# Performance work log

Measured on AMD Instinct MI355X. Metric: run time of the kernel, lower is better.

The kernel has to match this reference:

```python
import jax, jax.numpy as jnp
import numpy as np

N_NODES = 100000
N_EDGES = 1600000
IN_DIM, HID_DIM, OUT_DIM = 128, 128, 40
EPS = 1e-12


def setup_inputs() -> dict:
    key = jax.random.key(0)
    ks = jax.random.split(key, 7)
    x = jax.random.normal(ks[0], (N_NODES, IN_DIM), dtype=jnp.float32)
    edge_index = jax.random.randint(ks[1], (2, N_EDGES), 0, N_NODES, dtype=jnp.int64)
    s1 = 1.0 / np.sqrt(IN_DIM)
    s2 = 1.0 / np.sqrt(HID_DIM)
    return {
        "x": x,
        "edge_index": edge_index,
        "W1_l": jax.random.normal(ks[2], (HID_DIM, IN_DIM), dtype=jnp.float32) * s1,
        "b1": jnp.zeros((HID_DIM,), dtype=jnp.float32),
        "W1_r": jax.random.normal(ks[3], (HID_DIM, IN_DIM), dtype=jnp.float32) * s1,
        "W2_l": jax.random.normal(ks[4], (OUT_DIM, HID_DIM), dtype=jnp.float32) * s2,
        "b2": jnp.zeros((OUT_DIM,), dtype=jnp.float32),
        "W2_r": jax.random.normal(ks[5], (OUT_DIM, HID_DIM), dtype=jnp.float32) * s2,
    }


def _mean_aggregate(x, src, dst, deg_inv):
    # gather source features, scatter-sum into destination nodes, divide by degree
    summed = jax.ops.segment_sum(x[src], dst, num_segments=N_NODES)  # [N, d]
    return summed * deg_inv[:, None]


def _sage_conv(x, src, dst, deg_inv, W_l, b_l, W_r):
    # PyG SAGEConv(mean, normalize=True): lin_l(mean(x_j)) + lin_r(x_i), then L2-normalize
    agg = _mean_aggregate(x, src, dst, deg_inv)
    out = agg @ W_l.T + b_l + x @ W_r.T
    norm = jnp.sqrt(jnp.sum(out * out, axis=-1, keepdims=True))
    return out / jnp.maximum(norm, EPS)


def reference(x, edge_index, W1_l, b1, W1_r, W2_l, b2, W2_r):
    src, dst = edge_index[0], edge_index[1]
    deg = jax.ops.segment_sum(jnp.ones((src.shape[0],), dtype=x.dtype), dst,
                              num_segments=N_NODES)
    deg_inv = 1.0 / jnp.maximum(deg, 1.0)

    h = _sage_conv(x, src, dst, deg_inv, W1_l, b1, W1_r)
    h = jax.nn.relu(h)  # dropout = identity (deterministic reference)
    h = _sage_conv(h, src, dst, deg_inv, W2_l, b2, W2_r)
    h = jax.nn.relu(h)
    return jax.nn.log_softmax(h, axis=-1)
```

## Files before the change

### kernel.cpp

```cpp
#include <hip/hip_runtime.h>
#include <hip/hip_bf16.h>

#define N_NODES 100000
#define N_EDGES 1600000
#define IN_DIM 128
#define HID_DIM 128
#define OUT_DIM 40

#define BSHIFT 9
#define NBUCK 196
#define CHUNK 4096
#define NCHUNK ((N_EDGES + CHUNK - 1) / CHUNK)

typedef __attribute__((ext_vector_type(8))) short short8;
typedef __attribute__((ext_vector_type(4))) float float4v;
typedef __attribute__((ext_vector_type(2))) float f32x2;
typedef __attribute__((ext_vector_type(2))) unsigned int u32x2;
typedef __attribute__((ext_vector_type(4))) unsigned int u32x4;

typedef unsigned char u8;
typedef unsigned short u16;
typedef unsigned int u32;
typedef unsigned long long u64;

__device__ __forceinline__ float bflo(u32 v) { union { u32 u; float f; } c; c.u = v << 16; return c.f; }
__device__ __forceinline__ float bfhi(u32 v) { union { u32 u; float f; } c; c.u = v & 0xffff0000u; return c.f; }
__device__ __forceinline__ u16 f2bf(float f) {
    union { float f; u32 u; } c; c.f = f;
    u32 r = c.u + 0x7fffu + ((c.u >> 16) & 1u);
    return (u16)(r >> 16);
}
__device__ __forceinline__ u32 pk(float lo, float hi) {
    return ((u32)f2bf(hi) << 16) | (u32)f2bf(lo);
}

__device__ __forceinline__ u32 f2fp8(float f) {
    union { float f; u32 u; } c; c.f = f;
    u32 s = (c.u >> 24) & 0x80u;
    u32 a = c.u & 0x7fffffffu;
    u32 code;
    if (a >= 0x3C800000u) {
        if (a > 0x43E00000u) a = 0x43E00000u;
        u32 r = a + 0x0007FFFFu + ((a >> 20) & 1u);
        code = (((r >> 23) - 120u) << 3) | ((r >> 20) & 7u);
        if (code > 0x7Eu) code = 0x7Eu;
    } else {
        union { u32 u; float f; } d; d.u = a;
        code = (u32)(int)rintf(d.f * 512.0f);
    }
    return s | code;
}


#define XBLKS ((N_NODES * IN_DIM / 4 + 255) / 256)
#define WTRIP1 2048
#define WTRIP2 768
#define WBLKS 22

__global__ __launch_bounds__(256) void k_cvtall(
    const float* __restrict__ x, u16* __restrict__ xb, u32* __restrict__ xb8,
    const float* __restrict__ w1l, const float* __restrict__ w1r,
    const float* __restrict__ w2l, const float* __restrict__ w2r,
    u16* __restrict__ w1lf, u16* __restrict__ w1rf,
    u16* __restrict__ w2lf, u16* __restrict__ w2rf,
    const int* __restrict__ idx, int* __restrict__ bucket_size) {
    __shared__ int cnt[NBUCK];
    int b = blockIdx.x;
    if (b < XBLKS) {
        int i = b * 256 + threadIdx.x;
        if (i < N_NODES * IN_DIM / 4) {
            float4v v = reinterpret_cast<const float4v*>(x)[i];
            u32x2 o;
            o.x = pk(v.x, v.y);
            o.y = pk(v.z, v.w);
            reinterpret_cast<u32x2*>(xb)[i] = o;
            xb8[i] = f2fp8(v.x) | (f2fp8(v.y) << 8) | (f2fp8(v.z) << 16) | (f2fp8(v.w) << 24);
        }
        return;
    }
    if (b < XBLKS + WBLKS) {
        int i = (b - XBLKS) * 256 + threadIdx.x;
        const float* s; u16* d; int t; int rows;
        if (i < WTRIP1)            { s = w1l; d = w1lf; t = i;                 rows = HID_DIM; }
        else if (i < 2*WTRIP1)     { s = w1r; d = w1rf; t = i - WTRIP1;        rows = HID_DIM; }
        else if (i < 2*WTRIP1+WTRIP2)   { s = w2l; d = w2lf; t = i - 2*WTRIP1; rows = OUT_DIM; }
        else if (i < 2*WTRIP1+2*WTRIP2) { s = w2r; d = w2rf; t = i - 2*WTRIP1-WTRIP2; rows = OUT_DIM; }
        else return;
        int lane = t & 63;
        int ks = (t >> 6) & 3;
        int ct = t >> 8;
        int row = ct * 16 + (lane & 15);
        int col = ks * 32 + (lane >> 4) * 8;
        u32x4 o;
        if (row < rows) {
            const float* sp = s + row * 128 + col;
            float4v v0 = *reinterpret_cast<const float4v*>(sp);
            float4v v1 = *reinterpret_cast<const float4v*>(sp + 4);
            o.x = pk(v0.x, v0.y); o.y = pk(v0.z, v0.w);
            o.z = pk(v1.x, v1.y); o.w = pk(v1.z, v1.w);
        } else { o.x = 0; o.y = 0; o.z = 0; o.w = 0; }
        reinterpret_cast<u32x4*>(d)[t] = o;
        return;
    }
    int t = threadIdx.x;
    for (int i = t; i < NBUCK; i += 256) cnt[i] = 0;
    __syncthreads();
    int base = (b - XBLKS - WBLKS) * CHUNK;
    int n = min(CHUNK, N_EDGES - base);
    for (int i = t; i < n; i += 256)
        atomicAdd(&cnt[idx[N_EDGES + base + i] >> BSHIFT], 1);
    __syncthreads();
    for (int i = t; i < NBUCK; i += 256)
        if (cnt[i]) atomicAdd(&bucket_size[i], cnt[i]);
}


__global__ __launch_bounds__(1024) void k_bscatter(const int* __restrict__ idx,
                                                   const int* __restrict__ bucket_size,
                                                   int* __restrict__ bucket_cur,
                                                   u64* __restrict__ rec) {
    __shared__ int cnt[NBUCK], gbase[NBUCK];
    __shared__ int sa[256], sb[256];
    int t = threadIdx.x;
    const int nt = 1024;
    for (int i = t; i < NBUCK; i += nt) cnt[i] = 0;
    __syncthreads();
    int base = blockIdx.x * CHUNK;
    int n = min(CHUNK, N_EDGES - base);
    int eb[4], eq[4];
    u64 er[4];
    #pragma unroll
    for (int k = 0; k < 4; ++k) {
        int i = t + k * nt;
        if (i < n) {
            int srcv = idx[base + i];
            int dstv = idx[N_EDGES + base + i];
            int b = dstv >> BSHIFT;
            eb[k] = b;
            eq[k] = atomicAdd(&cnt[b], 1);
            er[k] = ((u64)(u32)dstv << 32) | (u32)srcv;
        }
    }
    int myv = 0;
    if (t < 256) {
        myv = (t < NBUCK) ? bucket_size[t] : 0;
        sa[t] = myv;
    }
    __syncthreads();
    int *s = sa, *d = sb;
    for (int dd = 1; dd < 256; dd <<= 1) {
        if (t < 256) d[t] = s[t] + ((t >= dd) ? s[t - dd] : 0);
        __syncthreads();
        int* tm = s; s = d; d = tm;
    }
    if (t < NBUCK) {
        int v = cnt[t];
        gbase[t] = v ? (s[t] - myv) + atomicAdd(&bucket_cur[t], v) : 0;
    }
    __syncthreads();
    #pragma unroll
    for (int k = 0; k < 4; ++k) {
        int i = t + k * nt;
        if (i < n) rec[gbase[eb[k]] + eq[k]] = er[k];
    }
}

__global__ __launch_bounds__(1024) void k_bfill(const u64* __restrict__ rec,
                                                const int* __restrict__ bucket_size,
                                                int* __restrict__ row_start,
                                                int* __restrict__ csr) {
    __shared__ int deg[512], cur[512];
    __shared__ int sa[512], sb[512];
    int t = threadIdx.x;
    int nt = blockDim.x;
    int b = blockIdx.x;
    int node0 = b << BSHIFT;
    int nn = min(512, N_NODES - node0);
    int esz = bucket_size[b];
    if (t < 256) sa[t] = (t < NBUCK) ? bucket_size[t] : 0;
    __syncthreads();
    {
        int *s = sa, *d = sb;
        for (int dd = 1; dd < 256; dd <<= 1) {
            if (t < 256) d[t] = s[t] + ((t >= dd) ? s[t - dd] : 0);
            __syncthreads();
            int* tm = s; s = d; d = tm;
        }
        if (t == 0) cur[0] = s[b] - esz;
    }
    __syncthreads();
    int ebase = cur[0];
    __syncthreads();
    for (int i = t; i < 512; i += nt) deg[i] = 0;
    __syncthreads();
    for (int i = t; i < esz; i += nt)
        atomicAdd(&deg[((int)(rec[ebase + i] >> 32)) & 511], 1);
    __syncthreads();
    for (int i = t; i < 512; i += nt) sa[i] = deg[i];
    __syncthreads();
    int *s = sa, *d = sb;
    for (int dd = 1; dd < 512; dd <<= 1) {
        for (int i = t; i < 512; i += nt) d[i] = s[i] + ((i >= dd) ? s[i - dd] : 0);
        __syncthreads();
        int* tm = s; s = d; d = tm;
    }
    for (int i = t; i < 512; i += nt) {
        int excl = s[i] - deg[i];
        cur[i] = excl;
        if (i < nn) row_start[node0 + i] = ebase + excl;
    }
    if (b == NBUCK - 1 && t == 0) row_start[N_NODES] = N_EDGES;
    __syncthreads();
    for (int i = t; i < esz; i += nt) {
        u64 r = rec[ebase + i];
        int dl = ((int)(r >> 32)) & 511;
        int p = atomicAdd(&cur[dl], 1);
        csr[ebase + p] = (int)(r & 0xffffffffu);
    }
}


__global__ void k_agg(const u32x2* __restrict__ fp,
                      const int* __restrict__ csr,
                      const int* __restrict__ row_start,
                      u16* __restrict__ agg) {
    int lane = threadIdx.x & 63;
    int wave = threadIdx.x >> 6;
    int sub = lane >> 4;
    int li = lane & 15;
    int n = blockIdx.x * 16 + wave * 4 + sub;
    int s = row_start[n];
    int e = row_start[n + 1];
    f32x2 ac0 = {0.f, 0.f}, ac1 = {0.f, 0.f}, ac2 = {0.f, 0.f}, ac3 = {0.f, 0.f};
#define ACC8(v) do { \
        ac0 += __builtin_amdgcn_cvt_pk_f32_fp8((v).x, false); \
        ac1 += __builtin_amdgcn_cvt_pk_f32_fp8((v).x, true);  \
        ac2 += __builtin_amdgcn_cvt_pk_f32_fp8((v).y, false); \
        ac3 += __builtin_amdgcn_cvt_pk_f32_fp8((v).y, true);  \
    } while (0)
    int p = s;
    int i0 = 0, i1 = 0;
    if (p + 2 <= e) { i0 = csr[p]; i1 = csr[p + 1]; }
    while (p + 2 <= e) {
        u32x2 v0 = fp[i0 * 16 + li];
        u32x2 v1 = fp[i1 * 16 + li];
        p += 2;
        if (p + 2 <= e) { i0 = csr[p]; i1 = csr[p + 1]; }
        ACC8(v0);
        ACC8(v1);
    }
    if (p < e) { u32x2 v = fp[csr[p] * 16 + li]; ACC8(v); }
#undef ACC8
    float sc = 1.0f / (float)max(e - s, 1);
    u32x4 o;
    o.x = pk(ac0.x * sc, ac0.y * sc);
    o.y = pk(ac1.x * sc, ac1.y * sc);
    o.z = pk(ac2.x * sc, ac2.y * sc);
    o.w = pk(ac3.x * sc, ac3.y * sc);
    *reinterpret_cast<u32x4*>(agg + n * 128 + li * 8) = o;
}


__global__ __launch_bounds__(256) void k_dense1(
    const u16* __restrict__ agg, const u16* __restrict__ x,
    const u16* __restrict__ W1lf, const u16* __restrict__ W1rf,
    const float* __restrict__ b1, u16* __restrict__ h) {
    __shared__ short8 wsh[2][WTRIP1];
    int t = threadIdx.x;
    int wave = t >> 6;
    int lane = t & 63;
    int nb = blockIdx.x * 64 + wave * 16;
    int q = lane >> 4;
    int m = lane & 15;
    int arow = nb + m;
    if (arow >= N_NODES) arow = N_NODES - 1;

    short8 afr[8];
    #pragma unroll
    for (int ks = 0; ks < 4; ++ks) {
        afr[ks]     = *reinterpret_cast<const short8*>(agg + arow * 128 + ks * 32 + q * 8);
        afr[4 + ks] = *reinterpret_cast<const short8*>(x   + arow * 128 + ks * 32 + q * 8);
    }
    const short8* g0 = reinterpret_cast<const short8*>(W1lf);
    const short8* g1 = reinterpret_cast<const short8*>(W1rf);
    #pragma unroll
    for (int k = 0; k < 8; ++k) {
        wsh[0][t + k * 256] = g0[t + k * 256];
        wsh[1][t + k * 256] = g1[t + k * 256];
    }
    __syncthreads();

    float4v acc[8];
    #pragma unroll
    for (int ct = 0; ct < 8; ++ct) acc[ct] = (float4v){0.f, 0.f, 0.f, 0.f};

    #pragma unroll
    for (int half = 0; half < 2; ++half)
        #pragma unroll
        for (int ks = 0; ks < 4; ++ks) {
            short8 a = afr[half * 4 + ks];
            #pragma unroll
            for (int ct = 0; ct < 8; ++ct) {
                short8 b = wsh[half][(ct * 4 + ks) * 64 + lane];
                acc[ct] = __builtin_amdgcn_mfma_f32_16x16x32_bf16(a, b, acc[ct], 0, 0, 0);
            }
        }

    float bias[8];
    #pragma unroll
    for (int ct = 0; ct < 8; ++ct) bias[ct] = b1[ct * 16 + m];

    float nsq[4] = { 0.f, 0.f, 0.f, 0.f };
    #pragma unroll
    for (int ct = 0; ct < 8; ++ct)
        #pragma unroll
        for (int r = 0; r < 4; ++r) {
            float v = acc[ct][r] + bias[ct];
            acc[ct][r] = v;
            nsq[r] += v * v;
        }
    #pragma unroll
    for (int r = 0; r < 4; ++r) {
        float tt = nsq[r];
        tt += __shfl_xor(tt, 1);
        tt += __shfl_xor(tt, 2);
        tt += __shfl_xor(tt, 4);
        tt += __shfl_xor(tt, 8);
        nsq[r] = 1.0f / fmaxf(sqrtf(tt), 1e-12f);
    }
    #pragma unroll
    for (int r = 0; r < 4; ++r) {
        int node = nb + q * 4 + r;
        if (node < N_NODES) {
            #pragma unroll
            for (int ct = 0; ct < 8; ++ct) {
                float v = fmaxf(acc[ct][r] * nsq[r], 0.0f);
                h[node * 128 + ct * 16 + m] = f2bf(v);
            }
        }
    }
}


__global__ __launch_bounds__(256) void k_dense2a(
    const u16* __restrict__ h,
    const u16* __restrict__ W2lf, const u16* __restrict__ W2rf,
    u8* __restrict__ y2, u16* __restrict__ z) {
    __shared__ short8 wsh[2][WTRIP2];
    int t = threadIdx.x;
    int wave = t >> 6;
    int lane = t & 63;
    int nb = blockIdx.x * 64 + wave * 16;
    int q = lane >> 4;
    int m = lane & 15;
    int arow = nb + m;
    if (arow >= N_NODES) arow = N_NODES - 1;

    short8 afr[4];
    #pragma unroll
    for (int ks = 0; ks < 4; ++ks)
        afr[ks] = *reinterpret_cast<const short8*>(h + arow * 128 + ks * 32 + q * 8);
    const short8* g0 = reinterpret_cast<const short8*>(W2lf);
    const short8* g1 = reinterpret_cast<const short8*>(W2rf);
    #pragma unroll
    for (int k = 0; k < 3; ++k) {
        wsh[0][t + k * 256] = g0[t + k * 256];
        wsh[1][t + k * 256] = g1[t + k * 256];
    }
    __syncthreads();

    float4v accl[3], accr[3];
    #pragma unroll
    for (int ct = 0; ct < 3; ++ct) {
        accl[ct] = (float4v){0.f, 0.f, 0.f, 0.f};
        accr[ct] = (float4v){0.f, 0.f, 0.f, 0.f};
    }
    #pragma unroll
    for (int ks = 0; ks < 4; ++ks) {
        short8 a = afr[ks];
        #pragma unroll
        for (int ct = 0; ct < 3; ++ct) {
            accl[ct] = __builtin_amdgcn_mfma_f32_16x16x32_bf16(a, wsh[0][(ct * 4 + ks) * 64 + lane], accl[ct], 0, 0, 0);
            accr[ct] = __builtin_amdgcn_mfma_f32_16x16x32_bf16(a, wsh[1][(ct * 4 + ks) * 64 + lane], accr[ct], 0, 0, 0);
        }
    }
    #pragma unroll
    for (int r = 0; r < 4; ++r) {
        int node = nb + q * 4 + r;
        if (node < N_NODES) {
            #pragma unroll
            for (int ct = 0; ct < 3; ++ct) {
                int col = ct * 16 + m;
                y2[node * 64 + col] = (u8)f2fp8(accl[ct][r] * 64.0f);
                z[node * 48 + col]  = f2bf(accr[ct][r]);
            }
            y2[node * 64 + 48 + m] = 0;
        }
    }
}


__global__ void k_agg2(const u32x2* __restrict__ fp,
                       const int* __restrict__ csr,
                       const int* __restrict__ row_start,
                       const u16* __restrict__ z,
                       const float* __restrict__ b2,
                       float* __restrict__ out) {
    int lane = threadIdx.x & 63;
    int wave = threadIdx.x >> 6;
    int sub = lane >> 3;
    int li = lane & 7;
    int n = blockIdx.x * 32 + wave * 8 + sub;
    int s = row_start[n];
    int e = row_start[n + 1];
    f32x2 ac0 = {0.f, 0.f}, ac1 = {0.f, 0.f}, ac2 = {0.f, 0.f}, ac3 = {0.f, 0.f};
#define ACC8(v) do { \
        ac0 += __builtin_amdgcn_cvt_pk_f32_fp8((v).x, false); \
        ac1 += __builtin_amdgcn_cvt_pk_f32_fp8((v).x, true);  \
        ac2 += __builtin_amdgcn_cvt_pk_f32_fp8((v).y, false); \
        ac3 += __builtin_amdgcn_cvt_pk_f32_fp8((v).y, true);  \
    } while (0)
    int p = s;
    int i0 = 0, i1 = 0;
    if (p + 2 <= e) { i0 = csr[p]; i1 = csr[p + 1]; }
    while (p + 2 <= e) {
        u32x2 v0 = fp[i0 * 8 + li];
        u32x2 v1 = fp[i1 * 8 + li];
        p += 2;
        if (p + 2 <= e) { i0 = csr[p]; i1 = csr[p + 1]; }
        ACC8(v0);
        ACC8(v1);
    }
    if (p < e) { u32x2 v = fp[csr[p] * 8 + li]; ACC8(v); }
#undef ACC8
    float a[8] = { ac0.x, ac0.y, ac1.x, ac1.y, ac2.x, ac2.y, ac3.x, ac3.y };

    float sc = 1.0f / (64.0f * (float)max(e - s, 1));
    float v[8];
    if (li < 5) {
        u32x4 zv = *reinterpret_cast<const u32x4*>(z + n * 48 + li * 8);
        float4v bv0 = *reinterpret_cast<const float4v*>(b2 + li * 8);
        float4v bv1 = *reinterpret_cast<const float4v*>(b2 + li * 8 + 4);
        v[0] = a[0] * sc + bflo(zv.x) + bv0.x;
        v[1] = a[1] * sc + bfhi(zv.x) + bv0.y;
        v[2] = a[2] * sc + bflo(zv.y) + bv0.z;
        v[3] = a[3] * sc + bfhi(zv.y) + bv0.w;
        v[4] = a[4] * sc + bflo(zv.z) + bv1.x;
        v[5] = a[5] * sc + bfhi(zv.z) + bv1.y;
        v[6] = a[6] * sc + bflo(zv.w) + bv1.z;
        v[7] = a[7] * sc + bfhi(zv.w) + bv1.w;
    } else {
        #pragma unroll
        for (int j = 0; j < 8; ++j) v[j] = 0.f;
    }
    float nsq = 0.f;
    #pragma unroll
    for (int j = 0; j < 8; ++j) nsq += v[j] * v[j];
    nsq += __shfl_xor(nsq, 1);
    nsq += __shfl_xor(nsq, 2);
    nsq += __shfl_xor(nsq, 4);
    float rn = 1.0f / fmaxf(sqrtf(nsq), 1e-12f);
    float mv = 0.f;
    #pragma unroll
    for (int j = 0; j < 8; ++j) {
        v[j] = fmaxf(v[j] * rn, 0.f);
        mv = fmaxf(mv, v[j]);
    }
    mv = fmaxf(mv, __shfl_xor(mv, 1));
    mv = fmaxf(mv, __shfl_xor(mv, 2));
    mv = fmaxf(mv, __shfl_xor(mv, 4));
    float se = 0.f;
    if (li < 5) {
        #pragma unroll
        for (int j = 0; j < 8; ++j) se += __expf(v[j] - mv);
    }
    se += __shfl_xor(se, 1);
    se += __shfl_xor(se, 2);
    se += __shfl_xor(se, 4);
    float lse = __logf(se);
    if (li < 5) {
        float4v o0 = { v[0] - mv - lse, v[1] - mv - lse, v[2] - mv - lse, v[3] - mv - lse };
        float4v o1 = { v[4] - mv - lse, v[5] - mv - lse, v[6] - mv - lse, v[7] - mv - lse };
        *reinterpret_cast<float4v*>(out + n * OUT_DIM + li * 8) = o0;
        *reinterpret_cast<float4v*>(out + n * OUT_DIM + li * 8 + 4) = o1;
    }
}


extern "C" void kernel_launch(void* const* d_in, const int* in_sizes, int n_in,
                              void* d_out, int out_size, void* d_ws, size_t ws_size,
                              hipStream_t stream) {
    const float* x   = (const float*)d_in[0];
    const int*   idx = (const int*)d_in[1];
    const float* W1l = (const float*)d_in[2];
    const float* b1  = (const float*)d_in[3];
    const float* W1r = (const float*)d_in[4];
    const float* W2l = (const float*)d_in[5];
    const float* b2  = (const float*)d_in[6];
    const float* W2r = (const float*)d_in[7];
    float* out = (float*)d_out;

    char* ws = (char*)d_ws;
    int*   bucket_size = (int*)(ws + 0);
    int*   bucket_cur  = (int*)(ws + 1024);
    int*   row_start   = (int*)(ws + 16384);
    int*   csr         = (int*)(ws + 1216384);
    u16*   xb          = (u16*)(ws + 7616512);
    u8*    y2          = (u8*)(ws + 7616512);
    u16*   z           = (u16*)(ws + 20416512);
    u16*   agg         = (u16*)(ws + 33216512);
    u64*   rec         = (u64*)(ws + 58816512);
    u32*   xb8         = (u32*)(ws + 71616512);
    u16*   h           = (u16*)(ws + 58816512);
    u16*   W1lf        = (u16*)(ws + 84416512);
    u16*   W1rf        = (u16*)(ws + 84449280);
    u16*   W2lf        = (u16*)(ws + 84482048);
    u16*   W2rf        = (u16*)(ws + 84494336);

    hipMemsetAsync(ws, 0, 1808, stream);

    k_cvtall<<<XBLKS + WBLKS + NCHUNK, 256, 0, stream>>>(
        x, xb, xb8, W1l, W1r, W2l, W2r, W1lf, W1rf, W2lf, W2rf, idx, bucket_size);

    k_bscatter<<<NCHUNK, 1024, 0, stream>>>(idx, bucket_size, bucket_cur, rec);
    k_bfill<<<NBUCK, 1024, 0, stream>>>(rec, bucket_size, row_start, csr);

    k_agg<<<N_NODES / 16, 256, 0, stream>>>((const u32x2*)xb8, csr, row_start, agg);
    k_dense1<<<(N_NODES + 63) / 64, 256, 0, stream>>>(agg, xb, W1lf, W1rf, b1, h);
    k_dense2a<<<(N_NODES + 63) / 64, 256, 0, stream>>>(h, W2lf, W2rf, y2, z);
    k_agg2<<<N_NODES / 32, 256, 0, stream>>>((const u32x2*)y2, csr, row_start, z, b2, out);
}
```

Baseline: 249.0 us.

## Fuse dense layers, deepen gather prefetch, read weights from global directly

```diff
diff --git a/kernel.cpp b/kernel.cpp
--- a/kernel.cpp
+++ b/kernel.cpp
@@ -74,7 +74,9 @@
             o.x = pk(v.x, v.y);
             o.y = pk(v.z, v.w);
             reinterpret_cast<u32x2*>(xb)[i] = o;
-            xb8[i] = f2fp8(v.x) | (f2fp8(v.y) << 8) | (f2fp8(v.z) << 16) | (f2fp8(v.w) << 24);
+            u32 r8 = (u32)__builtin_amdgcn_cvt_pk_fp8_f32(v.x, v.y, 0, false);
+            r8 = (u32)__builtin_amdgcn_cvt_pk_fp8_f32(v.z, v.w, (int)r8, true);
+            xb8[i] = r8;
         }
         return;
     }
@@ -90,14 +92,24 @@
         int ks = (t >> 6) & 3;
         int ct = t >> 8;
         int row = ct * 16 + (lane & 15);
-        int col = ks * 32 + (lane >> 4) * 8;
         u32x4 o;
         if (row < rows) {
-            const float* sp = s + row * 128 + col;
-            float4v v0 = *reinterpret_cast<const float4v*>(sp);
-            float4v v1 = *reinterpret_cast<const float4v*>(sp + 4);
-            o.x = pk(v0.x, v0.y); o.y = pk(v0.z, v0.w);
-            o.z = pk(v1.x, v1.y); o.w = pk(v1.z, v1.w);
+            const float* sp = s + row * 128;
+            if (rows == HID_DIM) {
+                int col = ks * 32 + (lane >> 4) * 8;
+                float4v v0 = *reinterpret_cast<const float4v*>(sp + col);
+                float4v v1 = *reinterpret_cast<const float4v*>(sp + col + 4);
+                o.x = pk(v0.x, v0.y); o.y = pk(v0.z, v0.w);
+                o.z = pk(v1.x, v1.y); o.w = pk(v1.z, v1.w);
+            } else {
+                int c0 = ks * 4 + (lane >> 4);
+                float f0 = sp[c0];       float f1 = sp[c0 + 16];
+                float f2 = sp[c0 + 32];  float f3 = sp[c0 + 48];
+                float f4 = sp[c0 + 64];  float f5 = sp[c0 + 80];
+                float f6 = sp[c0 + 96];  float f7 = sp[c0 + 112];
+                o.x = pk(f0, f1); o.y = pk(f2, f3);
+                o.z = pk(f4, f5); o.w = pk(f6, f7);
+            }
         } else { o.x = 0; o.y = 0; o.z = 0; o.w = 0; }
         reinterpret_cast<u32x4*>(d)[t] = o;
         return;
@@ -239,17 +251,22 @@
         ac3 += __builtin_amdgcn_cvt_pk_f32_fp8((v).y, true);  \
     } while (0)
     int p = s;
-    int i0 = 0, i1 = 0;
-    if (p + 2 <= e) { i0 = csr[p]; i1 = csr[p + 1]; }
-    while (p + 2 <= e) {
-        u32x2 v0 = fp[i0 * 16 + li];
-        u32x2 v1 = fp[i1 * 16 + li];
-        p += 2;
-        if (p + 2 <= e) { i0 = csr[p]; i1 = csr[p + 1]; }
-        ACC8(v0);
-        ACC8(v1);
-    }
-    if (p < e) { u32x2 v = fp[csr[p] * 16 + li]; ACC8(v); }
+    u32x2 v0, v1, v2, v3;
+    if (p + 4 <= e) {
+        int j0 = csr[p], j1 = csr[p + 1], j2 = csr[p + 2], j3 = csr[p + 3];
+        v0 = fp[j0 * 16 + li]; v1 = fp[j1 * 16 + li];
+        v2 = fp[j2 * 16 + li]; v3 = fp[j3 * 16 + li];
+    }
+    while (p + 8 <= e) {
+        int k0 = csr[p + 4], k1 = csr[p + 5], k2 = csr[p + 6], k3 = csr[p + 7];
+        u32x2 w0 = fp[k0 * 16 + li], w1 = fp[k1 * 16 + li];
+        u32x2 w2 = fp[k2 * 16 + li], w3 = fp[k3 * 16 + li];
+        ACC8(v0); ACC8(v1); ACC8(v2); ACC8(v3);
+        v0 = w0; v1 = w1; v2 = w2; v3 = w3;
+        p += 4;
+    }
+    if (p + 4 <= e) { ACC8(v0); ACC8(v1); ACC8(v2); ACC8(v3); p += 4; }
+    while (p < e) { u32x2 v = fp[csr[p] * 16 + li]; ACC8(v); ++p; }
 #undef ACC8
     float sc = 1.0f / (float)max(e - s, 1);
     u32x4 o;
@@ -261,11 +278,13 @@
 }
 
 
-__global__ __launch_bounds__(256) void k_dense1(
+__global__ __launch_bounds__(256) void k_dense(
     const u16* __restrict__ agg, const u16* __restrict__ x,
     const u16* __restrict__ W1lf, const u16* __restrict__ W1rf,
-    const float* __restrict__ b1, u16* __restrict__ h) {
-    __shared__ short8 wsh[2][WTRIP1];
+    const u16* __restrict__ W2lf, const u16* __restrict__ W2rf,
+    const float* __restrict__ b1,
+    u8* __restrict__ y2, u16* __restrict__ z) {
+    __shared__ short8 hbuf[4][4][64];
     int t = threadIdx.x;
     int wave = t >> 6;
     int lane = t & 63;
@@ -283,28 +302,24 @@
     }
     const short8* g0 = reinterpret_cast<const short8*>(W1lf);
     const short8* g1 = reinterpret_cast<const short8*>(W1rf);
-    #pragma unroll
-    for (int k = 0; k < 8; ++k) {
-        wsh[0][t + k * 256] = g0[t + k * 256];
-        wsh[1][t + k * 256] = g1[t + k * 256];
-    }
-    __syncthreads();
 
     float4v acc[8];
     #pragma unroll
     for (int ct = 0; ct < 8; ++ct) acc[ct] = (float4v){0.f, 0.f, 0.f, 0.f};
 
     #pragma unroll
-    for (int half = 0; half < 2; ++half)
+    for (int half = 0; half < 2; ++half) {
+        const short8* g = half ? g1 : g0;
         #pragma unroll
         for (int ks = 0; ks < 4; ++ks) {
             short8 a = afr[half * 4 + ks];
             #pragma unroll
             for (int ct = 0; ct < 8; ++ct) {
-                short8 b = wsh[half][(ct * 4 + ks) * 64 + lane];
-                acc[ct] = __builtin_amdgcn_mfma_f32_16x16x32_bf16(a, b, acc[ct], 0, 0, 0);
+                short8 bfrag = g[(ct * 4 + ks) * 64 + lane];
+                acc[ct] = __builtin_amdgcn_mfma_f32_16x16x32_bf16(a, bfrag, acc[ct], 0, 0, 0);
             }
         }
+    }
 
     float bias[8];
     #pragma unroll
@@ -330,45 +345,19 @@
     }
     #pragma unroll
     for (int r = 0; r < 4; ++r) {
-        int node = nb + q * 4 + r;
-        if (node < N_NODES) {
-            #pragma unroll
-            for (int ct = 0; ct < 8; ++ct) {
-                float v = fmaxf(acc[ct][r] * nsq[r], 0.0f);
-                h[node * 128 + ct * 16 + m] = f2bf(v);
-            }
-        }
-    }
-}
-
-
-__global__ __launch_bounds__(256) void k_dense2a(
-    const u16* __restrict__ h,
-    const u16* __restrict__ W2lf, const u16* __restrict__ W2rf,
-    u8* __restrict__ y2, u16* __restrict__ z) {
-    __shared__ short8 wsh[2][WTRIP2];
-    int t = threadIdx.x;
-    int wave = t >> 6;
-    int lane = t & 63;
-    int nb = blockIdx.x * 64 + wave * 16;
-    int q = lane >> 4;
-    int m = lane & 15;
-    int arow = nb + m;
-    if (arow >= N_NODES) arow = N_NODES - 1;
-
-    short8 afr[4];
-    #pragma unroll
-    for (int ks = 0; ks < 4; ++ks)
-        afr[ks] = *reinterpret_cast<const short8*>(h + arow * 128 + ks * 32 + q * 8);
-    const short8* g0 = reinterpret_cast<const short8*>(W2lf);
-    const short8* g1 = reinterpret_cast<const short8*>(W2rf);
-    #pragma unroll
-    for (int k = 0; k < 3; ++k) {
-        wsh[0][t + k * 256] = g0[t + k * 256];
-        wsh[1][t + k * 256] = g1[t + k * 256];
-    }
-    __syncthreads();
-
+        short8 hs;
+        #pragma unroll
+        for (int ct = 0; ct < 8; ++ct)
+            hs[ct] = (short)f2bf(fmaxf(acc[ct][r] * nsq[r], 0.0f));
+        hbuf[wave][m >> 2][(m & 3) * 16 + q * 4 + r] = hs;
+    }
+
+    short8 a2[4];
+    #pragma unroll
+    for (int ks = 0; ks < 4; ++ks) a2[ks] = hbuf[wave][ks][lane];
+
+    const short8* h0 = reinterpret_cast<const short8*>(W2lf);
+    const short8* h1 = reinterpret_cast<const short8*>(W2rf);
     float4v accl[3], accr[3];
     #pragma unroll
     for (int ct = 0; ct < 3; ++ct) {
@@ -377,11 +366,11 @@
     }
     #pragma unroll
     for (int ks = 0; ks < 4; ++ks) {
-        short8 a = afr[ks];
+        short8 a = a2[ks];
         #pragma unroll
         for (int ct = 0; ct < 3; ++ct) {
-            accl[ct] = __builtin_amdgcn_mfma_f32_16x16x32_bf16(a, wsh[0][(ct * 4 + ks) * 64 + lane], accl[ct], 0, 0, 0);
-            accr[ct] = __builtin_amdgcn_mfma_f32_16x16x32_bf16(a, wsh[1][(ct * 4 + ks) * 64 + lane], accr[ct], 0, 0, 0);
+            accl[ct] = __builtin_amdgcn_mfma_f32_16x16x32_bf16(a, h0[(ct * 4 + ks) * 64 + lane], accl[ct], 0, 0, 0);
+            accr[ct] = __builtin_amdgcn_mfma_f32_16x16x32_bf16(a, h1[(ct * 4 + ks) * 64 + lane], accr[ct], 0, 0, 0);
         }
     }
     #pragma unroll
@@ -421,17 +410,22 @@
         ac3 += __builtin_amdgcn_cvt_pk_f32_fp8((v).y, true);  \
     } while (0)
     int p = s;
-    int i0 = 0, i1 = 0;
-    if (p + 2 <= e) { i0 = csr[p]; i1 = csr[p + 1]; }
-    while (p + 2 <= e) {
-        u32x2 v0 = fp[i0 * 8 + li];
-        u32x2 v1 = fp[i1 * 8 + li];
-        p += 2;
-        if (p + 2 <= e) { i0 = csr[p]; i1 = csr[p + 1]; }
-        ACC8(v0);
-        ACC8(v1);
-    }
-    if (p < e) { u32x2 v = fp[csr[p] * 8 + li]; ACC8(v); }
+    u32x2 v0, v1, v2, v3;
+    if (p + 4 <= e) {
+        int j0 = csr[p], j1 = csr[p + 1], j2 = csr[p + 2], j3 = csr[p + 3];
+        v0 = fp[j0 * 8 + li]; v1 = fp[j1 * 8 + li];
+        v2 = fp[j2 * 8 + li]; v3 = fp[j3 * 8 + li];
+    }
+    while (p + 8 <= e) {
+        int k0 = csr[p + 4], k1 = csr[p + 5], k2 = csr[p + 6], k3 = csr[p + 7];
+        u32x2 w0 = fp[k0 * 8 + li], w1 = fp[k1 * 8 + li];
+        u32x2 w2 = fp[k2 * 8 + li], w3 = fp[k3 * 8 + li];
+        ACC8(v0); ACC8(v1); ACC8(v2); ACC8(v3);
+        v0 = w0; v1 = w1; v2 = w2; v3 = w3;
+        p += 4;
+    }
+    if (p + 4 <= e) { ACC8(v0); ACC8(v1); ACC8(v2); ACC8(v3); p += 4; }
+    while (p < e) { u32x2 v = fp[csr[p] * 8 + li]; ACC8(v); ++p; }
 #undef ACC8
     float a[8] = { ac0.x, ac0.y, ac1.x, ac1.y, ac2.x, ac2.y, ac3.x, ac3.y };
 
@@ -506,12 +500,11 @@
     int*   row_start   = (int*)(ws + 16384);
     int*   csr         = (int*)(ws + 1216384);
     u16*   xb          = (u16*)(ws + 7616512);
-    u8*    y2          = (u8*)(ws + 7616512);
-    u16*   z           = (u16*)(ws + 20416512);
-    u16*   agg         = (u16*)(ws + 33216512);
+    u16*   aggb        = (u16*)(ws + 33216512);
     u64*   rec         = (u64*)(ws + 58816512);
     u32*   xb8         = (u32*)(ws + 71616512);
-    u16*   h           = (u16*)(ws + 58816512);
+    u8*    y2          = (u8*)(ws + 58816512);
+    u16*   z           = (u16*)(ws + 65216512);
     u16*   W1lf        = (u16*)(ws + 84416512);
     u16*   W1rf        = (u16*)(ws + 84449280);
     u16*   W2lf        = (u16*)(ws + 84482048);
@@ -525,8 +518,7 @@
     k_bscatter<<<NCHUNK, 1024, 0, stream>>>(idx, bucket_size, bucket_cur, rec);
     k_bfill<<<NBUCK, 1024, 0, stream>>>(rec, bucket_size, row_start, csr);
 
-    k_agg<<<N_NODES / 16, 256, 0, stream>>>((const u32x2*)xb8, csr, row_start, agg);
-    k_dense1<<<(N_NODES + 63) / 64, 256, 0, stream>>>(agg, xb, W1lf, W1rf, b1, h);
-    k_dense2a<<<(N_NODES + 63) / 64, 256, 0, stream>>>(h, W2lf, W2rf, y2, z);
+    k_agg<<<N_NODES / 16, 256, 0, stream>>>((const u32x2*)xb8, csr, row_start, aggb);
+    k_dense<<<(N_NODES + 63) / 64, 256, 0, stream>>>(aggb, xb, W1lf, W1rf, W2lf, W2rf, b1, y2, z);
     k_agg2<<<N_NODES / 32, 256, 0, stream>>>((const u32x2*)y2, csr, row_start, z, b2, out);
 }
```

Result: faster. 241.0 us (-3.2%).
